# Kernel tuning notes

Hardware: AMD Instinct MI355X
Metric: run time of the kernel (lower is better)

The kernel has to match this reference:

```python
import jax, jax.numpy as jnp
import numpy as np

N_NODES = 100000
N_EDGES = 1600000
D_IN = 256
D_OUT = 128


def setup_inputs() -> dict:
    key = jax.random.key(0)
    k1, k2, k3, k4, k5, k6 = jax.random.split(key, 6)
    x = jax.random.normal(k1, (N_NODES, D_IN), dtype=jnp.float32)
    src = jax.random.randint(k2, (N_EDGES,), 0, N_NODES, dtype=jnp.int64)
    dst = jnp.sort(jax.random.randint(k3, (N_EDGES,), 0, N_NODES, dtype=jnp.int64))
    w = jax.random.uniform(k4, (N_EDGES,), dtype=jnp.float32)
    # nn.Linear(input_size, output_size): weight [out, in], bias [out]
    bound = 1.0 / np.sqrt(D_IN)
    W = jax.random.uniform(k5, (D_OUT, D_IN), dtype=jnp.float32, minval=-bound, maxval=bound)
    b = jax.random.uniform(k6, (D_OUT,), dtype=jnp.float32, minval=-bound, maxval=bound)
    return {"x": x, "src": src, "dst": dst, "w": w, "W": W, "b": b}


def reference(x, src, dst, w, W, b):
    # h = linear(x)
    h = jnp.einsum("ni,oi->no", x, W) + b  # [N, D_OUT]
    # u_mul_e: message m_e = h[src_e] * w_e ; sum: out[v] = sum_{e: dst_e=v} m_e
    msgs = h[src] * w[:, None]  # [E, D_OUT]
    out = jax.ops.segment_sum(msgs, dst, num_segments=N_NODES)
    return out
```

## Files before the change

kernel.cpp:

```cpp
#include <hip/hip_runtime.h>

#define N_NODES 100000
#define N_EDGES 1600000
#define D_IN    256
#define D_OUT   128

typedef __attribute__((ext_vector_type(8))) short          bf16x8;
typedef __attribute__((ext_vector_type(8))) unsigned short ushort8;
typedef __attribute__((ext_vector_type(4))) float          f32x4;

__device__ inline unsigned short f2bf(float f) {
  union { float f; unsigned u; } v; v.f = f;
  unsigned r = v.u + 0x7fffu + ((v.u >> 16) & 1u);
  return (unsigned short)(r >> 16);
}
__device__ inline float bf2f(unsigned short u) {
  union { unsigned u; float f; } v; v.u = ((unsigned)u) << 16;
  return v.f;
}

__global__ __launch_bounds__(256) void gcn_packW_kernel(
    const float* __restrict__ W, unsigned short* __restrict__ Wp) {
  int f = blockIdx.x * blockDim.x + threadIdx.x;
  if (f >= 4096) return;
  int n = f >> 9, s = (f >> 6) & 7, lane = f & 63;
  int col = n * 16 + (lane & 15);
  int k0  = s * 32 + (lane >> 4) * 8;
#pragma unroll
  for (int j = 0; j < 8; ++j)
    Wp[f * 8 + j] = f2bf(W[col * D_IN + k0 + j]);
}

__global__ __launch_bounds__(512) void gcn_linear_mfma_kernel(
    const float* __restrict__ x, const unsigned short* __restrict__ Wp,
    const float* __restrict__ b, unsigned short* __restrict__ h) {
  __shared__ unsigned short lW[32768];
  const int tid  = threadIdx.x;
  const int lane = tid & 63;
  const int wid  = tid >> 6;
  const int r0   = blockIdx.x * 128 + wid * 16;

#pragma unroll
  for (int i = 0; i < 8; ++i) {
    int idx = i * 512 + tid;
    *(ushort8*)(&lW[idx * 8]) = *(const ushort8*)(Wp + (size_t)idx * 8);
  }
  __syncthreads();

  int arow = r0 + (lane & 15);
  arow = arow < N_NODES ? arow : N_NODES - 1;
  const int kg = (lane >> 4) * 8;
  const float* xrow = x + (size_t)arow * D_IN + kg;

  f32x4 acc[8];
#pragma unroll
  for (int n = 0; n < 8; ++n) acc[n] = (f32x4){0.f, 0.f, 0.f, 0.f};

#pragma unroll
  for (int s = 0; s < 8; ++s) {
    float4 a0 = *(const float4*)(xrow + s * 32);
    float4 a1 = *(const float4*)(xrow + s * 32 + 4);
    bf16x8 af;
    af[0] = (short)f2bf(a0.x); af[1] = (short)f2bf(a0.y);
    af[2] = (short)f2bf(a0.z); af[3] = (short)f2bf(a0.w);
    af[4] = (short)f2bf(a1.x); af[5] = (short)f2bf(a1.y);
    af[6] = (short)f2bf(a1.z); af[7] = (short)f2bf(a1.w);
#pragma unroll
    for (int n = 0; n < 8; ++n) {
      bf16x8 bfrag = *(const bf16x8*)(&lW[(size_t)((n * 8 + s) * 64 + lane) * 8]);
      acc[n] = __builtin_amdgcn_mfma_f32_16x16x32_bf16(af, bfrag, acc[n], 0, 0, 0);
    }
  }

  const int col0 = lane & 15;
  const int q4   = (lane >> 4) * 4;
#pragma unroll
  for (int n = 0; n < 8; ++n) {
    const int col = n * 16 + col0;
    const float bias = b[col];
#pragma unroll
    for (int i = 0; i < 4; ++i) {
      const int row = r0 + q4 + i;
      if (row < N_NODES)
        h[(size_t)row * D_OUT + col] = f2bf(acc[n][i] + bias);
    }
  }
}

__global__ __launch_bounds__(256) void gcn_rowptr_kernel(
    const int* __restrict__ dst, int* __restrict__ row_ptr) {
  int v = blockIdx.x * blockDim.x + threadIdx.x;
  if (v > N_NODES) return;
  int lo = 0, hi = N_EDGES;
  while (lo < hi) {
    int mid = (lo + hi) >> 1;
    if (dst[mid] < v) lo = mid + 1; else hi = mid;
  }
  row_ptr[v] = lo;
}

__global__ __launch_bounds__(256) void gcn_agg_kernel(
    const unsigned short* __restrict__ h, const int* __restrict__ src,
    const float* __restrict__ w, const int* __restrict__ rp,
    float* __restrict__ out) {
  const int node = (blockIdx.x << 2) + (threadIdx.x >> 6);
  if (node >= N_NODES) return;
  const int lane = threadIdx.x & 63;
  const int g  = lane >> 4;
  const int dg = (lane & 15) << 3;

  const int s = rp[node], e = rp[node + 1];
  float acc[8];
#pragma unroll
  for (int j = 0; j < 8; ++j) acc[j] = 0.f;

  for (int base = s; base < e; base += 16) {
    const int i0 = base + (g << 2);
    if (i0 < e) {
      int   sv[4];
      float wv[4];
#pragma unroll
      for (int j = 0; j < 4; ++j) {
        int  i = i0 + j;
        bool valid = (i < e);
        int  ic = valid ? i : i0;
        sv[j] = src[ic];
        wv[j] = valid ? w[ic] : 0.f;
      }
      ushort8 hv[4];
#pragma unroll
      for (int j = 0; j < 4; ++j)
        hv[j] = *(const ushort8*)(h + (size_t)sv[j] * D_OUT + dg);
#pragma unroll
      for (int j = 0; j < 4; ++j)
#pragma unroll
        for (int k = 0; k < 8; ++k)
          acc[k] += bf2f(hv[j][k]) * wv[j];
    }
  }

#pragma unroll
  for (int j = 0; j < 8; ++j) acc[j] += __shfl_xor(acc[j], 16);
#pragma unroll
  for (int j = 0; j < 8; ++j) acc[j] += __shfl_xor(acc[j], 32);

  if (g == 0) {
    float4 o0 = {acc[0], acc[1], acc[2], acc[3]};
    float4 o1 = {acc[4], acc[5], acc[6], acc[7]};
    float* op = out + (size_t)node * D_OUT + dg;
    *(float4*)(op)     = o0;
    *(float4*)(op + 4) = o1;
  }
}

extern "C" void kernel_launch(void* const* d_in, const int* in_sizes, int n_in,
                              void* d_out, int out_size, void* d_ws, size_t ws_size,
                              hipStream_t stream) {
  const float* x   = (const float*)d_in[0];
  const int*   src = (const int*)d_in[1];
  const int*   dst = (const int*)d_in[2];
  const float* w   = (const float*)d_in[3];
  const float* W   = (const float*)d_in[4];
  const float* b   = (const float*)d_in[5];
  float* out = (float*)d_out;

  unsigned short* Wp = (unsigned short*)d_ws;
  unsigned short* h  = (unsigned short*)((char*)d_ws + 65536);
  int* row_ptr = (int*)((char*)d_ws + 65536 + (size_t)N_NODES * D_OUT * sizeof(unsigned short));

  gcn_packW_kernel<<<16, 256, 0, stream>>>(W, Wp);
  gcn_rowptr_kernel<<<(N_NODES + 1 + 255) / 256, 256, 0, stream>>>(dst, row_ptr);
  gcn_linear_mfma_kernel<<<(N_NODES + 127) / 128, 512, 0, stream>>>(x, Wp, b, h);
  gcn_agg_kernel<<<N_NODES / 4, 256, 0, stream>>>(h, src, w, row_ptr, out);
}
```

Baseline: 110.7 us.

## Fuse prep kernels, split linear GEMM by output half, stage stores through LDS

Merges the W-packing and row_ptr binary-search kernels into a single launch, which removes one kernel launch. The linear MFMA kernel now splits the 128 output columns across two blocks, so each block holds half the packed W in LDS (32 KB) and half the accumulators, and the launch bounds ask for higher occupancy. Results are staged through LDS so h is written as coalesced 16-byte stores instead of scattered 2-byte stores. The cost is that each x row is now read and converted to bf16 twice, and extra barriers are added.

Result: no change. 110.6 us (-0.2%).

```diff
diff --git a/kernel.cpp b/kernel.cpp
--- a/kernel.cpp
+++ b/kernel.cpp
@@ -19,31 +19,45 @@
   return v.f;
 }
 
-__global__ __launch_bounds__(256) void gcn_packW_kernel(
-    const float* __restrict__ W, unsigned short* __restrict__ Wp) {
-  int f = blockIdx.x * blockDim.x + threadIdx.x;
-  if (f >= 4096) return;
-  int n = f >> 9, s = (f >> 6) & 7, lane = f & 63;
-  int col = n * 16 + (lane & 15);
-  int k0  = s * 32 + (lane >> 4) * 8;
+__global__ __launch_bounds__(256) void gcn_prep_kernel(
+    const float* __restrict__ W, unsigned short* __restrict__ Wp,
+    const int* __restrict__ dst, int* __restrict__ row_ptr) {
+  int gid = blockIdx.x * blockDim.x + threadIdx.x;
+  if (gid < 4096) {
+    int f = gid;
+    int n = f >> 9, s = (f >> 6) & 7, lane = f & 63;
+    int col = n * 16 + (lane & 15);
+    int k0  = s * 32 + (lane >> 4) * 8;
 #pragma unroll
-  for (int j = 0; j < 8; ++j)
-    Wp[f * 8 + j] = f2bf(W[col * D_IN + k0 + j]);
+    for (int j = 0; j < 8; ++j)
+      Wp[f * 8 + j] = f2bf(W[col * D_IN + k0 + j]);
+  } else {
+    int v = gid - 4096;
+    if (v > N_NODES) return;
+    int lo = 0, hi = N_EDGES;
+    while (lo < hi) {
+      int mid = (lo + hi) >> 1;
+      if (dst[mid] < v) lo = mid + 1; else hi = mid;
+    }
+    row_ptr[v] = lo;
+  }
 }
 
-__global__ __launch_bounds__(512) void gcn_linear_mfma_kernel(
+__global__ __launch_bounds__(512, 8) void gcn_linear_mfma_kernel(
     const float* __restrict__ x, const unsigned short* __restrict__ Wp,
     const float* __restrict__ b, unsigned short* __restrict__ h) {
-  __shared__ unsigned short lW[32768];
+  __shared__ unsigned short lW[16384];
   const int tid  = threadIdx.x;
   const int lane = tid & 63;
   const int wid  = tid >> 6;
-  const int r0   = blockIdx.x * 128 + wid * 16;
+  const int half = blockIdx.x & 1;
+  const int r0   = (blockIdx.x >> 1) * 128 + wid * 16;
 
 #pragma unroll
-  for (int i = 0; i < 8; ++i) {
+  for (int i = 0; i < 4; ++i) {
     int idx = i * 512 + tid;
-    *(ushort8*)(&lW[idx * 8]) = *(const ushort8*)(Wp + (size_t)idx * 8);
+    *(ushort8*)(&lW[idx * 8]) =
+        *(const ushort8*)(Wp + ((size_t)(half * 2048 + idx)) * 8);
   }
   __syncthreads();
 
@@ -52,9 +66,9 @@
   const int kg = (lane >> 4) * 8;
   const float* xrow = x + (size_t)arow * D_IN + kg;
 
-  f32x4 acc[8];
+  f32x4 acc[4];
 #pragma unroll
-  for (int n = 0; n < 8; ++n) acc[n] = (f32x4){0.f, 0.f, 0.f, 0.f};
+  for (int n = 0; n < 4; ++n) acc[n] = (f32x4){0.f, 0.f, 0.f, 0.f};
 
 #pragma unroll
   for (int s = 0; s < 8; ++s) {
@@ -66,37 +80,34 @@
     af[4] = (short)f2bf(a1.x); af[5] = (short)f2bf(a1.y);
     af[6] = (short)f2bf(a1.z); af[7] = (short)f2bf(a1.w);
 #pragma unroll
-    for (int n = 0; n < 8; ++n) {
+    for (int n = 0; n < 4; ++n) {
       bf16x8 bfrag = *(const bf16x8*)(&lW[(size_t)((n * 8 + s) * 64 + lane) * 8]);
       acc[n] = __builtin_amdgcn_mfma_f32_16x16x32_bf16(af, bfrag, acc[n], 0, 0, 0);
     }
   }
 
+  __syncthreads();
+  unsigned short* my = &lW[wid * 1024];
   const int col0 = lane & 15;
   const int q4   = (lane >> 4) * 4;
 #pragma unroll
-  for (int n = 0; n < 8; ++n) {
-    const int col = n * 16 + col0;
-    const float bias = b[col];
+  for (int n = 0; n < 4; ++n) {
+    const float bias = b[half * 64 + n * 16 + col0];
 #pragma unroll
-    for (int i = 0; i < 4; ++i) {
-      const int row = r0 + q4 + i;
-      if (row < N_NODES)
-        h[(size_t)row * D_OUT + col] = f2bf(acc[n][i] + bias);
+    for (int i = 0; i < 4; ++i)
+      my[(q4 + i) * 64 + n * 16 + col0] = f2bf(acc[n][i] + bias);
+  }
+  __syncthreads();
+#pragma unroll
+  for (int j = 0; j < 2; ++j) {
+    const int flat = j * 64 + lane;
+    const int row  = flat >> 3;
+    const int cin  = (flat & 7) * 8;
+    if (r0 + row < N_NODES) {
+      ushort8 v = *(const ushort8*)(&my[(size_t)flat * 8]);
+      *(ushort8*)(&h[(size_t)(r0 + row) * D_OUT + half * 64 + cin]) = v;
     }
   }
-}
-
-__global__ __launch_bounds__(256) void gcn_rowptr_kernel(
-    const int* __restrict__ dst, int* __restrict__ row_ptr) {
-  int v = blockIdx.x * blockDim.x + threadIdx.x;
-  if (v > N_NODES) return;
-  int lo = 0, hi = N_EDGES;
-  while (lo < hi) {
-    int mid = (lo + hi) >> 1;
-    if (dst[mid] < v) lo = mid + 1; else hi = mid;
-  }
-  row_ptr[v] = lo;
 }
 
 __global__ __launch_bounds__(256) void gcn_agg_kernel(
@@ -168,8 +179,7 @@
   unsigned short* h  = (unsigned short*)((char*)d_ws + 65536);
   int* row_ptr = (int*)((char*)d_ws + 65536 + (size_t)N_NODES * D_OUT * sizeof(unsigned short));
 
-  gcn_packW_kernel<<<16, 256, 0, stream>>>(W, Wp);
-  gcn_rowptr_kernel<<<(N_NODES + 1 + 255) / 256, 256, 0, stream>>>(dst, row_ptr);
-  gcn_linear_mfma_kernel<<<(N_NODES + 127) / 128, 512, 0, stream>>>(x, Wp, b, h);
+  gcn_prep_kernel<<<(4096 + N_NODES + 1 + 255) / 256, 256, 0, stream>>>(W, Wp, dst, row_ptr);
+  gcn_linear_mfma_kernel<<<2 * ((N_NODES + 127) / 128), 512, 0, stream>>>(x, Wp, b, h);
   gcn_agg_kernel<<<N_NODES / 4, 256, 0, stream>>>(h, src, w, row_ptr, out);
 }
```
